# Performance work log

Hardware: AMD Instinct MI355X
Metric: run time of the kernel (lower is better)

Reference implementation:

```python
import jax, jax.numpy as jnp
import numpy as np

B, T, DC, DM, R = 64, 1000, 512, 80, 1
DP = 128          # prenet output dim
DH = 128          # prenet hidden dim
DA = 128          # attention hidden dim
DR = (1024, 1024) # decoder LSTM hidden dims
PZ = 0.1          # zoneout prob (eval-mode mixing)
PD = 0.5          # prenet dropout prob (always on)


def setup_inputs() -> dict:
    key = jax.random.key(0)
    ks = jax.random.split(key, 24)
    s = 0.02  # weight scale to keep activations in a sane range
    inp = {}
    inp['x'] = jax.random.normal(ks[0], (B, R, DM), jnp.float32)
    w = jax.random.uniform(ks[1], (B, T), jnp.float32)
    inp['w'] = w / jnp.sum(w, axis=1, keepdims=True)  # valid attention weights
    inp['h0'] = jax.random.normal(ks[2], (B, DR[0]), jnp.float32) * 0.1
    inp['c0'] = jax.random.normal(ks[3], (B, DR[0]), jnp.float32) * 0.1
    inp['h1'] = jax.random.normal(ks[4], (B, DR[1]), jnp.float32) * 0.1
    inp['c1'] = jax.random.normal(ks[5], (B, DR[1]), jnp.float32) * 0.1
    inp['memory'] = jax.random.normal(ks[6], (B, T, DC), jnp.float32)
    inp['mmask'] = jnp.ones((B, T), dtype=bool)
    inp['pre_w1'] = jax.random.normal(ks[7], (DM * R, DH), jnp.float32) * s
    inp['pre_b1'] = jnp.zeros((DH,), jnp.float32)
    inp['pre_w2'] = jax.random.normal(ks[8], (DH, DP), jnp.float32) * s
    inp['pre_b2'] = jnp.zeros((DP,), jnp.float32)
    inp['wih0'] = jax.random.normal(ks[9], (DP + DC, 4 * DR[0]), jnp.float32) * s
    inp['whh0'] = jax.random.normal(ks[10], (DR[0], 4 * DR[0]), jnp.float32) * s
    inp['b0'] = jnp.zeros((4 * DR[0],), jnp.float32)
    inp['wih1'] = jax.random.normal(ks[11], (DR[0] + DC, 4 * DR[1]), jnp.float32) * s
    inp['whh1'] = jax.random.normal(ks[12], (DR[1], 4 * DR[1]), jnp.float32) * s
    inp['b1'] = jnp.zeros((4 * DR[1],), jnp.float32)
    inp['att_wq'] = jax.random.normal(ks[13], (DR[0] + DR[1] + DC, DA), jnp.float32) * s
    inp['att_wm'] = jax.random.normal(ks[14], (DC, DA), jnp.float32) * s
    inp['att_b'] = jnp.zeros((DA,), jnp.float32)
    inp['att_v'] = jax.random.normal(ks[15], (DA,), jnp.float32) * s
    return inp


def _dropout(v, k, p):
    keep = jax.random.bernoulli(k, 1.0 - p, v.shape)
    return jnp.where(keep, v / (1.0 - p), 0.0)


def _lstm_zoneout(xi, h, c, wih, whh, b):
    # torch LSTMCell gate order: i, f, g, o
    g = xi @ wih + h @ whh + b
    i, f, gg, o = jnp.split(g, 4, axis=1)
    c_new = jax.nn.sigmoid(f) * c + jax.nn.sigmoid(i) * jnp.tanh(gg)
    h_new = jax.nn.sigmoid(o) * jnp.tanh(c_new)
    # eval-mode zoneout: expected-value mixing with previous state
    return (1.0 - PZ) * h_new + PZ * h, (1.0 - PZ) * c_new + PZ * c


def reference(x, w, h0, c0, h1, c1, memory, pre_w1, pre_b1, pre_w2, pre_b2,
              wih0, whh0, b0, wih1, whh1, b1, att_wq, att_wm, att_b, att_v, mmask):
    dk = jax.random.split(jax.random.key(42), 2)
    # PreNet (dropout always on, fixed keys for determinism)
    xf = x.reshape(x.shape[0], -1)                       # [B, r*dim_mel]
    h = _dropout(jax.nn.relu(xf @ pre_w1 + pre_b1), dk[0], PD)
    x_pre = _dropout(jax.nn.relu(h @ pre_w2 + pre_b2), dk[1], PD)  # [B, DP]
    # context = bmm(w, memory)
    ctx = jnp.einsum('bt,btc->bc', w, memory)            # [B, DC]
    # stacked zoneout LSTM cells with interleaved context concat
    h0n, c0n = _lstm_zoneout(jnp.concatenate([x_pre, ctx], axis=1), h0, c0, wih0, whh0, b0)
    h1n, c1n = _lstm_zoneout(jnp.concatenate([h0n, ctx], axis=1), h1, c1, wih1, whh1, b1)
    x_att = jnp.concatenate([h0n, h1n, jnp.zeros_like(ctx)], axis=1)  # [B, 2560]
    # stepwise monotonic attention: e = v.tanh(Wq q + Wm m + b); p = sigmoid(e)
    q = x_att @ att_wq                                   # [B, DA]
    proc = jnp.tanh(q[:, None, :] + jnp.einsum('btc,ca->bta', memory, att_wm) + att_b)
    e = jnp.einsum('bta,a->bt', proc, att_v)             # [B, T]
    e = jnp.where(mmask, e, -1e9)
    p = jax.nn.sigmoid(e)
    # alpha_j = alpha_j * p_j + alpha_{j-1} * (1 - p_{j-1})
    w_new = w * p + jnp.pad((w * (1.0 - p))[:, :-1], ((0, 0), (1, 0)))
    x_dec = jnp.concatenate([h0n, h1n, jnp.zeros_like(ctx)], axis=1)
    return x_dec, ctx, w_new, h0n, c0n, h1n, c1n
```

## Files before the change

kernel.cpp:

```cpp
#include <hip/hip_runtime.h>
#include <hip/hip_bf16.h>
#include <stdint.h>

#define B_  64
#define T_  1000
#define DC_ 512
#define DM_ 80
#define DP_ 128
#define DH_ 128
#define DA_ 128
#define DRN 1024
#define G4  4096

typedef __hip_bfloat16 bf16;
typedef unsigned short u16;
typedef unsigned int   u32;

typedef short bf8_t __attribute__((ext_vector_type(8)));
typedef float f4_t  __attribute__((ext_vector_type(4)));

#define O_XDEC 0
#define O_CTX  163840
#define O_WN   196608
#define O_H0   260608
#define O_C0   326144
#define O_H1   391680
#define O_C1   457216

__device__ __forceinline__ float b2f(bf16 v) { return __bfloat162float(v); }
__device__ __forceinline__ bf16  f2b(float v) { return __float2bfloat16(v); }
__device__ __forceinline__ u16   f2bu(float v) { return __builtin_bit_cast(u16, __float2bfloat16(v)); }

__device__ __forceinline__ float ldv(const float* p, size_t i) { return p[i]; }
__device__ __forceinline__ float ldv(const bf16*  p, size_t i) { return b2f(p[i]); }
__device__ __forceinline__ void  stv(float* p, size_t i, float v) { p[i] = v; }
__device__ __forceinline__ void  stv(bf16*  p, size_t i, float v) { p[i] = f2b(v); }

template<typename T>
__device__ __forceinline__ void ld8f(const T* p, size_t i, float* o) {
    if constexpr (sizeof(T) == 2) {
        uint4 u = *(const uint4*)((const u16*)p + i);
        o[0] = __uint_as_float(u.x << 16); o[1] = __uint_as_float(u.x & 0xffff0000u);
        o[2] = __uint_as_float(u.y << 16); o[3] = __uint_as_float(u.y & 0xffff0000u);
        o[4] = __uint_as_float(u.z << 16); o[5] = __uint_as_float(u.z & 0xffff0000u);
        o[6] = __uint_as_float(u.w << 16); o[7] = __uint_as_float(u.w & 0xffff0000u);
    } else {
        float4 a = *(const float4*)(p + i);
        float4 b = *(const float4*)(p + i + 4);
        o[0]=a.x; o[1]=a.y; o[2]=a.z; o[3]=a.w; o[4]=b.x; o[5]=b.y; o[6]=b.z; o[7]=b.w;
    }
}
__device__ __forceinline__ void ld8f_bits(const u16* p, size_t i, float* o) {
    uint4 u = *(const uint4*)(p + i);
    o[0] = __uint_as_float(u.x << 16); o[1] = __uint_as_float(u.x & 0xffff0000u);
    o[2] = __uint_as_float(u.y << 16); o[3] = __uint_as_float(u.y & 0xffff0000u);
    o[4] = __uint_as_float(u.z << 16); o[5] = __uint_as_float(u.z & 0xffff0000u);
    o[6] = __uint_as_float(u.w << 16); o[7] = __uint_as_float(u.w & 0xffff0000u);
}

__device__ __forceinline__ bool sniff_is_f32(const u32* h0raw) {
    int lane = threadIdx.x & 63;
    int c = 0;
    #pragma unroll
    for (int i = 0; i < 4; ++i) {
        u32 e = (h0raw[lane * 4 + i] >> 7) & 0xFF;
        c += (e >= 100 && e <= 126) ? 1 : 0;
    }
    #pragma unroll
    for (int s = 1; s < 64; s <<= 1) c += __shfl_xor(c, s);
    return c < 128;
}

__device__ __forceinline__ u32 rotl32(u32 v, int r) { return (v << r) | (v >> (32 - r)); }
__device__ __forceinline__ void threefry2x32(u32 k0, u32 k1, u32 x0, u32 x1, u32& y0, u32& y1) {
    u32 ks2 = k0 ^ k1 ^ 0x1BD11BDAu;
    x0 += k0; x1 += k1;
#define TF_R(r) { x0 += x1; x1 = rotl32(x1, r); x1 ^= x0; }
    TF_R(13) TF_R(15) TF_R(26) TF_R(6)
    x0 += k1; x1 += ks2 + 1u;
    TF_R(17) TF_R(29) TF_R(16) TF_R(24)
    x0 += ks2; x1 += k0 + 2u;
    TF_R(13) TF_R(15) TF_R(26) TF_R(6)
    x0 += k0; x1 += k1 + 3u;
    TF_R(17) TF_R(29) TF_R(16) TF_R(24)
    x0 += k1; x1 += ks2 + 4u;
    TF_R(13) TF_R(15) TF_R(26) TF_R(6)
    x0 += ks2; x1 += k0 + 5u;
#undef TF_R
    y0 = x0; y1 = x1;
}
__device__ __forceinline__ float dropout_mask(int which, int j) {
    u32 dk0, dk1, b1, b2;
    threefry2x32(0u, 42u, 0u, (u32)which, dk0, dk1);
    threefry2x32(dk0, dk1, 0u, (u32)j, b1, b2);
    u32 bits = b1 ^ b2;
    float u = __uint_as_float((bits >> 9) | 0x3f800000u) - 1.0f;
    return (u < 0.5f) ? 2.0f : 0.0f;
}

template<typename T>
__device__ void prep_impl(const T* wm, u16* BTwm,
                          const T* x, const T* w1, const T* pb1, const T* w2, const T* pb2,
                          u16* Ab0, float* shbuf) {
    int bid = blockIdx.x, tid = threadIdx.x;
    if (bid < 32) {
        int gid = bid * 256 + tid;
        int L = gid & 63, kc = (gid >> 6) & 15, at = gid >> 10;
        u16* dst = BTwm + (size_t)gid * 8;
        int col = at * 16 + (L & 15);
        int krow = kc * 32 + (L >> 4) * 8;
        u16 v[8];
        #pragma unroll
        for (int j = 0; j < 8; ++j) v[j] = f2bu(ldv(wm, (size_t)(krow + j) * DA_ + col));
        uint4 pk;
        pk.x = v[0] | ((u32)v[1] << 16); pk.y = v[2] | ((u32)v[3] << 16);
        pk.z = v[4] | ((u32)v[5] << 16); pk.w = v[6] | ((u32)v[7] << 16);
        *(uint4*)dst = pk;
    } else {
        int b = bid - 32;
        float* xs = shbuf;
        float* hs = shbuf + DM_;
        if (tid < DM_) xs[tid] = ldv(x, (size_t)b * DM_ + tid);
        __syncthreads();
        if (tid < DH_) {
            float acc = ldv(pb1, tid);
            #pragma unroll 8
            for (int k = 0; k < DM_; ++k) acc = fmaf(xs[k], ldv(w1, (size_t)k * DH_ + tid), acc);
            acc = fmaxf(acc, 0.f) * dropout_mask(0, b * DH_ + tid);
            hs[tid] = acc;
        }
        __syncthreads();
        if (tid < DP_) {
            float acc2 = ldv(pb2, tid);
            #pragma unroll 8
            for (int k = 0; k < DH_; ++k) acc2 = fmaf(hs[k], ldv(w2, (size_t)k * DP_ + tid), acc2);
            acc2 = fmaxf(acc2, 0.f) * dropout_mask(1, b * DP_ + tid);
            Ab0[(size_t)b * 1664 + tid] = f2bu(acc2);
        }
    }
}
__global__ __launch_bounds__(256) void prep_kernel(const u32* h0r,
        const void* wm, u16* BTwm,
        const void* x, const void* w1, const void* pb1, const void* w2, const void* pb2,
        u16* Ab0) {
    __shared__ float shbuf[DM_ + DH_];
    if (sniff_is_f32(h0r))
        prep_impl<float>((const float*)wm, BTwm, (const float*)x,
                         (const float*)w1, (const float*)pb1, (const float*)w2, (const float*)pb2, Ab0, shbuf);
    else
        prep_impl<bf16>((const bf16*)wm, BTwm, (const bf16*)x,
                        (const bf16*)w1, (const bf16*)pb1, (const bf16*)w2, (const bf16*)pb2, Ab0, shbuf);
}

template<typename T>
__device__ void ctxproj_impl(const T* mem, const T* w, const u16* BTwm,
                             float* CTXP, u16* Mproj, u16* Alds, float* shw) {
    int tid = threadIdx.x;
    int t0 = blockIdx.x * 128, b = blockIdx.y;
    if (tid < 128) shw[tid] = (t0 + tid < T_) ? ldv(w, (size_t)b * T_ + t0 + tid) : 0.f;
    int L = tid & 63;
    int m = L & 15, q16 = L >> 4;
    int wat = tid >> 6;
    int rg = tid >> 5, cg = tid & 31;

    bf8_t bw[16];
    #pragma unroll
    for (int kc = 0; kc < 16; ++kc)
        bw[kc] = *(const bf8_t*)(BTwm + ((size_t)(wat * 16 + kc) * 64 + L) * 8);

    f4_t acc[4];
    #pragma unroll
    for (int mt = 0; mt < 4; ++mt) acc[mt] = (f4_t){0.f, 0.f, 0.f, 0.f};
    float cacc[16] = {};
    uint4  stb[4];
    float4 stf[8];

#define LOADSTEP(S) do {                                                         \
        const int tt_ = (S) >> 1, ph_ = (S) & 1;                                 \
        _Pragma("unroll")                                                        \
        for (int rr = 0; rr < 4; ++rr) {                                         \
            int i = rr * 512 + tid;                                              \
            int row = i >> 5, c16 = i & 31;                                      \
            int t = t0 + tt_ * 64 + row;                                         \
            size_t base = (size_t)(b * T_ + ((t < T_) ? t : 0)) * DC_ + ph_ * 256 + c16 * 8; \
            if constexpr (sizeof(T) == 2) {                                      \
                stb[rr] = (t < T_) ? *(const uint4*)((const u16*)mem + base)     \
                                   : make_uint4(0u, 0u, 0u, 0u);                 \
            } else {                                                             \
                if (t < T_) { stf[2*rr]   = *(const float4*)(mem + base);        \
                              stf[2*rr+1] = *(const float4*)(mem + base + 4); }  \
                else { stf[2*rr] = make_float4(0.f,0.f,0.f,0.f);                 \
                       stf[2*rr+1] = make_float4(0.f,0.f,0.f,0.f); }             \
            }                                                                    \
        }                                                                        \
    } while (0)

    LOADSTEP(0);
    #pragma unroll
    for (int step = 0; step < 4; ++step) {
        const int tt = step >> 1, ph = step & 1;
        __syncthreads();
        #pragma unroll
        for (int rr = 0; rr < 4; ++rr) {
            int i = rr * 512 + tid;
            int row = i >> 5, c16 = i & 31;
            float wvv = shw[tt * 64 + row];
            uint4 v;
            if constexpr (sizeof(T) == 2) {
                v = stb[rr];
                float f0 = __uint_as_float(v.x << 16), f1 = __uint_as_float(v.x & 0xffff0000u);
                float f2 = __uint_as_float(v.y << 16), f3 = __uint_as_float(v.y & 0xffff0000u);
                float f4 = __uint_as_float(v.z << 16), f5 = __uint_as_float(v.z & 0xffff0000u);
                float f6 = __uint_as_float(v.w << 16), f7 = __uint_as_float(v.w & 0xffff0000u);
                cacc[ph*8+0] = fmaf(wvv, f0, cacc[ph*8+0]); cacc[ph*8+1] = fmaf(wvv, f1, cacc[ph*8+1]);
                cacc[ph*8+2] = fmaf(wvv, f2, cacc[ph*8+2]); cacc[ph*8+3] = fmaf(wvv, f3, cacc[ph*8+3]);
                cacc[ph*8+4] = fmaf(wvv, f4, cacc[ph*8+4]); cacc[ph*8+5] = fmaf(wvv, f5, cacc[ph*8+5]);
                cacc[ph*8+6] = fmaf(wvv, f6, cacc[ph*8+6]); cacc[ph*8+7] = fmaf(wvv, f7, cacc[ph*8+7]);
            } else {
                float4 a = stf[2*rr], bb = stf[2*rr+1];
                cacc[ph*8+0] = fmaf(wvv, a.x,  cacc[ph*8+0]); cacc[ph*8+1] = fmaf(wvv, a.y,  cacc[ph*8+1]);
                cacc[ph*8+2] = fmaf(wvv, a.z,  cacc[ph*8+2]); cacc[ph*8+3] = fmaf(wvv, a.w,  cacc[ph*8+3]);
                cacc[ph*8+4] = fmaf(wvv, bb.x, cacc[ph*8+4]); cacc[ph*8+5] = fmaf(wvv, bb.y, cacc[ph*8+5]);
                cacc[ph*8+6] = fmaf(wvv, bb.z, cacc[ph*8+6]); cacc[ph*8+7] = fmaf(wvv, bb.w, cacc[ph*8+7]);
                v.x = (u32)f2bu(a.x)  | ((u32)f2bu(a.y)  << 16);
                v.y = (u32)f2bu(a.z)  | ((u32)f2bu(a.w)  << 16);
                v.z = (u32)f2bu(bb.x) | ((u32)f2bu(bb.y) << 16);
                v.w = (u32)f2bu(bb.z) | ((u32)f2bu(bb.w) << 16);
            }
            *(uint4*)(Alds + row * 264 + c16 * 8) = v;
        }
        __syncthreads();
        if (step == 0) LOADSTEP(1);
        else if (step == 1) LOADSTEP(2);
        else if (step == 2) LOADSTEP(3);
        #pragma unroll
        for (int kcl = 0; kcl < 8; ++kcl) {
            const int kc = ph * 8 + kcl;
            #pragma unroll
            for (int mt = 0; mt < 4; ++mt) {
                bf8_t af = *(const bf8_t*)(Alds + (mt * 16 + m) * 264 + kcl * 32 + q16 * 8);
                acc[mt] = __builtin_amdgcn_mfma_f32_16x16x32_bf16(af, bw[kc], acc[mt], 0, 0, 0);
            }
        }
        if (ph == 1) {
            #pragma unroll
            for (int mt = 0; mt < 4; ++mt) {
                #pragma unroll
                for (int r = 0; r < 4; ++r) {
                    int trow = t0 + tt * 64 + mt * 16 + q16 * 4 + r;
                    if (trow < T_)
                        Mproj[(size_t)(b * T_ + trow) * DA_ + wat * 16 + m] = f2bu(acc[mt][r]);
                }
                acc[mt] = (f4_t){0.f, 0.f, 0.f, 0.f};
            }
        }
    }
#undef LOADSTEP
    __syncthreads();
    float* part = (float*)Alds;
    #pragma unroll
    for (int ph = 0; ph < 2; ++ph)
        #pragma unroll
        for (int j = 0; j < 8; ++j)
            part[rg * 512 + ph * 256 + cg * 8 + j] = cacc[ph * 8 + j];
    __syncthreads();
    int c = tid;
    float s = 0.f;
    #pragma unroll
    for (int gg = 0; gg < 16; ++gg) s += part[gg * 512 + c];
    CTXP[((size_t)blockIdx.x * 64 + b) * DC_ + c] = s;
}
__global__ __launch_bounds__(512, 1) void ctxproj_bf16_kernel(const u32* h0r,
        const void* mem, const void* w, const u16* BTwm, float* CTXP, u16* Mproj) {
    __shared__ __align__(16) u16 Alds[64 * 264];
    __shared__ float shw[128];
    if (sniff_is_f32(h0r)) return;
    ctxproj_impl<bf16>((const bf16*)mem, (const bf16*)w, BTwm, CTXP, Mproj, Alds, shw);
}
__global__ __launch_bounds__(512, 1) void ctxproj_f32_kernel(const u32* h0r,
        const void* mem, const void* w, const u16* BTwm, float* CTXP, u16* Mproj) {
    __shared__ __align__(16) u16 Alds[64 * 264];
    __shared__ float shw[128];
    if (!sniff_is_f32(h0r)) return;
    ctxproj_impl<float>((const float*)mem, (const float*)w, BTwm, CTXP, Mproj, Alds, shw);
}

template<typename T>
__device__ void pack0_impl(const float* CTXP, const T* h0p, const T* h1p,
                           u16* Ab0, u16* Ab1, float* QPf, T* out) {
    int b = blockIdx.x, tid = threadIdx.x;
    T* ctxout = out + O_CTX;
    T* xdec = out + O_XDEC;
    if (tid < 128) QPf[(size_t)b * DA_ + tid] = 0.f;
    for (int c = tid; c < DC_; c += 256) {
        float s = 0.f;
        #pragma unroll
        for (int t = 0; t < 8; ++t) s += CTXP[((size_t)t * 64 + b) * DC_ + c];
        u16 bv = f2bu(s);
        Ab0[(size_t)b * 1664 + 128 + c] = bv;
        Ab1[(size_t)b * 2560 + 1024 + c] = bv;
        stv(ctxout, (size_t)b * DC_ + c, s);
        stv(xdec, (size_t)b * 2560 + 2048 + c, 0.f);
    }
    for (int u = tid; u < DRN; u += 256) {
        Ab0[(size_t)b * 1664 + 640 + u]  = f2bu(ldv(h0p, (size_t)b * DRN + u));
        Ab1[(size_t)b * 2560 + 1536 + u] = f2bu(ldv(h1p, (size_t)b * DRN + u));
    }
}
__global__ __launch_bounds__(256) void pack0_kernel(const u32* h0r, const float* CTXP,
        const void* h0p, const void* h1p, u16* Ab0, u16* Ab1, float* QPf, void* out) {
    if (sniff_is_f32(h0r))
        pack0_impl<float>(CTXP, (const float*)h0p, (const float*)h1p, Ab0, Ab1, QPf, (float*)out);
    else
        pack0_impl<bf16>(CTXP, (const bf16*)h0p, (const bf16*)h1p, Ab0, Ab1, QPf, (bf16*)out);
}

template<typename T>
__device__ void gemm_impl(const u16* Abuf, int K, int L12, const T* Wih, const T* Whh,
                          float* Gs, int nchunks, float (*As)[66], float (*Ws)[64]) {
    int tid = threadIdx.x;
    int n0b = blockIdx.x * 64;
    int kbase = blockIdx.y * (nchunks * 64);
    int cx = tid & 15, ry = tid >> 4;
    int b0 = ry * 4, n0 = cx * 4;
    int a_bb = tid >> 2, a_k16 = (tid & 3) * 16;
    int w_k  = tid >> 2, w_n16 = (tid & 3) * 16;
    float acc[4][4] = {};
    float va[16], vw[16];
#define GLOAD(CH) do {                                                          \
        int k0 = kbase + (CH) * 64;                                             \
        ld8f_bits(Abuf, (size_t)a_bb * K + k0 + a_k16, va);                     \
        ld8f_bits(Abuf, (size_t)a_bb * K + k0 + a_k16 + 8, va + 8);             \
        int kg = k0 + w_k;                                                      \
        const T* wr = (kg < L12) ? (Wih + (size_t)kg * G4) : (Whh + (size_t)(kg - L12) * G4); \
        ld8f(wr, n0b + w_n16, vw);                                              \
        ld8f(wr, n0b + w_n16 + 8, vw + 8);                                      \
    } while (0)
    GLOAD(0);
    for (int ch = 0; ch < nchunks; ++ch) {
        __syncthreads();
        #pragma unroll
        for (int j = 0; j < 16; ++j) As[a_bb][a_k16 + j] = va[j];
        #pragma unroll
        for (int j = 0; j < 16; ++j) Ws[w_k][w_n16 + j] = vw[j];
        __syncthreads();
        if (ch + 1 < nchunks) GLOAD(ch + 1);
        #pragma unroll
        for (int kk = 0; kk < 64; kk += 2) {
            float2 av[4];
            #pragma unroll
            for (int r = 0; r < 4; ++r) av[r] = *(const float2*)&As[b0 + r][kk];
            float4 w0 = *(const float4*)&Ws[kk][n0];
            float4 w1 = *(const float4*)&Ws[kk + 1][n0];
            #pragma unroll
            for (int r = 0; r < 4; ++r) {
                acc[r][0] = fmaf(av[r].x, w0.x, acc[r][0]); acc[r][0] = fmaf(av[r].y, w1.x, acc[r][0]);
                acc[r][1] = fmaf(av[r].x, w0.y, acc[r][1]); acc[r][1] = fmaf(av[r].y, w1.y, acc[r][1]);
                acc[r][2] = fmaf(av[r].x, w0.z, acc[r][2]); acc[r][2] = fmaf(av[r].y, w1.z, acc[r][2]);
                acc[r][3] = fmaf(av[r].x, w0.w, acc[r][3]); acc[r][3] = fmaf(av[r].y, w1.w, acc[r][3]);
            }
        }
    }
#undef GLOAD
    float* outp = Gs + (size_t)blockIdx.y * (64 * G4);
    #pragma unroll
    for (int r = 0; r < 4; ++r)
        *(float4*)&outp[(size_t)(b0 + r) * G4 + n0b + n0] =
            make_float4(acc[r][0], acc[r][1], acc[r][2], acc[r][3]);
}
__global__ __launch_bounds__(256) void gemm_kernel(const u32* h0r, const u16* Abuf,
        int K, int L12, const void* Wih, const void* Whh, float* Gs, int nchunks) {
    __shared__ float As[64][66];
    __shared__ float Ws[64][64];
    if (sniff_is_f32(h0r))
        gemm_impl<float>(Abuf, K, L12, (const float*)Wih, (const float*)Whh, Gs, nchunks, As, Ws);
    else
        gemm_impl<bf16>(Abuf, K, L12, (const bf16*)Wih, (const bf16*)Whh, Gs, nchunks, As, Ws);
}

template<typename T>
__device__ void gate_impl(const float* Gs, int nsplit, const T* bias, const T* hprev,
                          const T* cprev, const T* wq, int qrow0, float* QPf,
                          T* out, int ho_off, int co_off, int xoff, u16* Ab1,
                          float* hos, float* sarr) {
    int tid = threadIdx.x;
    int idx = blockIdx.x * 256 + tid;
    int b = idx >> 10, u = idx & 1023;
    int u0 = (blockIdx.x & 3) * 256;
    float gi = ldv(bias, u);
    float gf = ldv(bias, 1024 + u);
    float gg = ldv(bias, 2048 + u);
    float go = ldv(bias, 3072 + u);
    for (int s = 0; s < nsplit; ++s) {
        const float* g = Gs + (size_t)s * (64 * G4) + (size_t)b * G4;
        gi += g[u]; gf += g[1024 + u]; gg += g[2048 + u]; go += g[3072 + u];
    }
    float c = ldv(cprev, idx), h = ldv(hprev, idx);
    float si = 1.f / (1.f + expf(-gi));
    float sf = 1.f / (1.f + expf(-gf));
    float so = 1.f / (1.f + expf(-go));
    float cn = sf * c + si * tanhf(gg);
    float hn = so * tanhf(cn);
    float ho = 0.9f * hn + 0.1f * h;
    float co = 0.9f * cn + 0.1f * c;
    stv(out + ho_off, idx, ho);
    stv(out + co_off, idx, co);
    stv(out + O_XDEC, (size_t)b * 2560 + xoff + u, ho);
    if (Ab1 != nullptr) Ab1[(size_t)b * 2560 + u] = f2bu(ho);
    hos[tid] = ho;
    __syncthreads();
    int a = tid & 127, half = tid >> 7;
    float s = 0.f;
    #pragma unroll 8
    for (int j = 0; j < 128; ++j)
        s = fmaf(hos[half * 128 + j], ldv(wq, (size_t)(qrow0 + u0 + half * 128 + j) * DA_ + a), s);
    sarr[tid] = s;
    __syncthreads();
    if (tid < 128) atomicAdd(&QPf[(size_t)b * DA_ + tid], sarr[tid] + sarr[128 + tid]);
}
__global__ __launch_bounds__(256) void gate_kernel(const u32* h0r, const float* Gs, int nsplit,
        const void* bias, const void* hprev, const void* cprev, const void* wq, int qrow0,
        float* QPf, void* out, int ho_off, int co_off, int xoff, u16* Ab1) {
    __shared__ float hos[256];
    __shared__ float sarr[256];
    if (sniff_is_f32(h0r))
        gate_impl<float>(Gs, nsplit, (const float*)bias, (const float*)hprev, (const float*)cprev,
                         (const float*)wq, qrow0, QPf, (float*)out, ho_off, co_off, xoff, Ab1, hos, sarr);
    else
        gate_impl<bf16>(Gs, nsplit, (const bf16*)bias, (const bf16*)hprev, (const bf16*)cprev,
                        (const bf16*)wq, qrow0, QPf, (bf16*)out, ho_off, co_off, xoff, Ab1, hos, sarr);
}

template<typename T>
__device__ void attn_impl(const u16* Mproj, const float* QPf, const T* ab, const T* av,
                          const T* w, T* out, float* qa, float* avl, float* psh) {
    int tid = threadIdx.x;
    int t0 = blockIdx.x * 64, b = blockIdx.y;
    T* wout = out + O_WN;
    if (tid < DA_) {
        qa[tid]  = ldv(ab, tid) + QPf[(size_t)b * DA_ + tid];
        avl[tid] = ldv(av, tid);
    }
    __syncthreads();
    int quad = tid & 3, r = tid >> 2;
    #pragma unroll
    for (int rbase = 0; rbase < 2; ++rbase) {
        int rrow = (rbase == 0) ? r : 64;
        bool act = (rbase == 0) || (r == 0);
        int t = t0 - 1 + rrow;
        float e = 0.f;
        if (act && t >= 0 && t < T_) {
            #pragma unroll
            for (int a8 = 0; a8 < 4; ++a8) {
                float v[8];
                ld8f_bits(Mproj, (size_t)(b * T_ + t) * DA_ + quad * 32 + a8 * 8, v);
                #pragma unroll
                for (int j = 0; j < 8; ++j) {
                    int a = quad * 32 + a8 * 8 + j;
                    e = fmaf(avl[a], tanhf(qa[a] + v[j]), e);
                }
            }
        }
        e += __shfl_xor(e, 1);
        e += __shfl_xor(e, 2);
        if (act && quad == 0 && t >= 0 && t < T_) psh[rrow] = 1.f / (1.f + expf(-e));
    }
    __syncthreads();
    if (tid < 64) {
        int t = t0 + tid;
        if (t < T_) {
            float val = ldv(w, (size_t)b * T_ + t) * psh[tid + 1];
            if (t > 0) val = fmaf(ldv(w, (size_t)b * T_ + t - 1), 1.f - psh[tid], val);
            stv(wout, (size_t)b * T_ + t, val);
        }
    }
}
__global__ __launch_bounds__(256) void attn_kernel(const u32* h0r, const u16* Mproj,
        const float* QPf, const void* ab, const void* av, const void* w, void* out) {
    __shared__ float qa[DA_];
    __shared__ float avl[DA_];
    __shared__ float psh[66];
    if (sniff_is_f32(h0r))
        attn_impl<float>(Mproj, QPf, (const float*)ab, (const float*)av, (const float*)w,
                         (float*)out, qa, avl, psh);
    else
        attn_impl<bf16>(Mproj, QPf, (const bf16*)ab, (const bf16*)av, (const bf16*)w,
                        (bf16*)out, qa, avl, psh);
}

extern "C" void kernel_launch(void* const* d_in, const int* in_sizes, int n_in,
                              void* d_out, int out_size, void* d_ws, size_t ws_size,
                              hipStream_t stream) {
    (void)in_sizes; (void)n_in; (void)out_size; (void)ws_size;

    float* wsf   = (float*)d_ws;
    float* GS    = wsf;
    float* CTXP  = wsf + 4194304;
    float* QPf   = wsf + 4718592;
    u16*   MPROJ = (u16*)(wsf + 4784128);
    u16*   AB0   = (u16*)(wsf + 8880128);
    u16*   AB1   = (u16*)(wsf + 8933376);
    u16*   BTWM  = (u16*)(wsf + 9080832);

    const u32* H0R = (const u32*)d_in[2];

    prep_kernel<<<96, 256, 0, stream>>>(H0R, d_in[19], BTWM,
                                        d_in[0], d_in[8], d_in[9], d_in[10], d_in[11], AB0);
    ctxproj_bf16_kernel<<<dim3(8, 64), 512, 0, stream>>>(H0R, d_in[6], d_in[1], BTWM, CTXP, MPROJ);
    ctxproj_f32_kernel <<<dim3(8, 64), 512, 0, stream>>>(H0R, d_in[6], d_in[1], BTWM, CTXP, MPROJ);
    pack0_kernel<<<64, 256, 0, stream>>>(H0R, CTXP, d_in[2], d_in[4], AB0, AB1, QPf, d_out);
    gemm_kernel<<<dim3(64, 13), 256, 0, stream>>>(H0R, AB0, 1664, 640, d_in[12], d_in[13], GS, 2);
    gate_kernel<<<256, 256, 0, stream>>>(H0R, GS, 13, d_in[14], d_in[2], d_in[3],
                                         d_in[18], 0, QPf, d_out, O_H0, O_C0, 0, AB1);
    gemm_kernel<<<dim3(64, 10), 256, 0, stream>>>(H0R, AB1, 2560, 1536, d_in[15], d_in[16], GS, 4);
    gate_kernel<<<256, 256, 0, stream>>>(H0R, GS, 10, d_in[17], d_in[4], d_in[5],
                                         d_in[18], 1024, QPf, d_out, O_H1, O_C1, 1024, (u16*)nullptr);
    attn_kernel<<<dim3(16, 64), 256, 0, stream>>>(H0R, MPROJ, QPf, d_in[20], d_in[21], d_in[1], d_out);
}
```

Baseline: 384.5 us.

## Precompute recurrent h@Whh GEMMs in prep kernel and double-buffer ctxproj loads

```diff
diff --git a/kernel.cpp b/kernel.cpp
--- a/kernel.cpp
+++ b/kernel.cpp
@@ -11,6 +11,7 @@
 #define DA_ 128
 #define DRN 1024
 #define G4  4096
+#define SPLIT 262144
 
 typedef __hip_bfloat16 bf16;
 typedef unsigned short u16;
@@ -99,9 +100,64 @@
 }
 
 template<typename T>
+__device__ void hgemm_impl(const T* hprev, const T* Whh, float* GsL, int unit,
+                           float (*As)[66], float (*Ws)[64]) {
+    int tid = threadIdx.x;
+    int n0b = (unit & 63) * 64;
+    int split = unit >> 6;
+    int kbase = split * 256;
+    int cx = tid & 15, ry = tid >> 4;
+    int b0 = ry * 4, n0 = cx * 4;
+    int a_bb = tid >> 2, a_k16 = (tid & 3) * 16;
+    int w_k  = tid >> 2, w_n16 = (tid & 3) * 16;
+    float acc[4][4] = {};
+    float va[16], vw[16];
+#define HGLOAD(CH) do {                                                         \
+        int k0 = kbase + (CH) * 64;                                             \
+        ld8f(hprev, (size_t)a_bb * DRN + k0 + a_k16, va);                       \
+        ld8f(hprev, (size_t)a_bb * DRN + k0 + a_k16 + 8, va + 8);               \
+        const T* wr = Whh + (size_t)(k0 + w_k) * G4;                            \
+        ld8f(wr, n0b + w_n16, vw);                                              \
+        ld8f(wr, n0b + w_n16 + 8, vw + 8);                                      \
+    } while (0)
+    HGLOAD(0);
+    for (int ch = 0; ch < 4; ++ch) {
+        __syncthreads();
+        #pragma unroll
+        for (int j = 0; j < 16; ++j) As[a_bb][a_k16 + j] = va[j];
+        #pragma unroll
+        for (int j = 0; j < 16; ++j) Ws[w_k][w_n16 + j] = vw[j];
+        __syncthreads();
+        if (ch + 1 < 4) HGLOAD(ch + 1);
+        #pragma unroll
+        for (int kk = 0; kk < 64; kk += 2) {
+            float2 av[4];
+            #pragma unroll
+            for (int r = 0; r < 4; ++r) av[r] = *(const float2*)&As[b0 + r][kk];
+            float4 w0 = *(const float4*)&Ws[kk][n0];
+            float4 w1 = *(const float4*)&Ws[kk + 1][n0];
+            #pragma unroll
+            for (int r = 0; r < 4; ++r) {
+                acc[r][0] = fmaf(av[r].x, w0.x, acc[r][0]); acc[r][0] = fmaf(av[r].y, w1.x, acc[r][0]);
+                acc[r][1] = fmaf(av[r].x, w0.y, acc[r][1]); acc[r][1] = fmaf(av[r].y, w1.y, acc[r][1]);
+                acc[r][2] = fmaf(av[r].x, w0.z, acc[r][2]); acc[r][2] = fmaf(av[r].y, w1.z, acc[r][2]);
+                acc[r][3] = fmaf(av[r].x, w0.w, acc[r][3]); acc[r][3] = fmaf(av[r].y, w1.w, acc[r][3]);
+            }
+        }
+    }
+#undef HGLOAD
+    float* outp = GsL + (size_t)split * (64 * G4);
+    #pragma unroll
+    for (int r = 0; r < 4; ++r)
+        *(float4*)&outp[(size_t)(b0 + r) * G4 + n0b + n0] =
+            make_float4(acc[r][0], acc[r][1], acc[r][2], acc[r][3]);
+}
+
+template<typename T>
 __device__ void prep_impl(const T* wm, u16* BTwm,
                           const T* x, const T* w1, const T* pb1, const T* w2, const T* pb2,
-                          u16* Ab0, float* shbuf) {
+                          u16* Ab0, const T* h0p, const T* whh0, const T* h1p, const T* whh1,
+                          float* GS, float (*As)[66], float (*Ws)[64]) {
     int bid = blockIdx.x, tid = threadIdx.x;
     if (bid < 32) {
         int gid = bid * 256 + tid;
@@ -116,10 +172,10 @@
         pk.x = v[0] | ((u32)v[1] << 16); pk.y = v[2] | ((u32)v[3] << 16);
         pk.z = v[4] | ((u32)v[5] << 16); pk.w = v[6] | ((u32)v[7] << 16);
         *(uint4*)dst = pk;
-    } else {
+    } else if (bid < 96) {
         int b = bid - 32;
-        float* xs = shbuf;
-        float* hs = shbuf + DM_;
+        float* xs = &As[0][0];
+        float* hs = xs + DM_;
         if (tid < DM_) xs[tid] = ldv(x, (size_t)b * DM_ + tid);
         __syncthreads();
         if (tid < DH_) {
@@ -137,19 +193,29 @@
             acc2 = fmaxf(acc2, 0.f) * dropout_mask(1, b * DP_ + tid);
             Ab0[(size_t)b * 1664 + tid] = f2bu(acc2);
         }
+    } else if (bid < 352) {
+        hgemm_impl<T>(h0p, whh0, GS, bid - 96, As, Ws);
+    } else {
+        hgemm_impl<T>(h1p, whh1, GS + (size_t)6 * SPLIT, bid - 352, As, Ws);
     }
 }
 __global__ __launch_bounds__(256) void prep_kernel(const u32* h0r,
         const void* wm, u16* BTwm,
         const void* x, const void* w1, const void* pb1, const void* w2, const void* pb2,
-        u16* Ab0) {
-    __shared__ float shbuf[DM_ + DH_];
+        u16* Ab0, const void* h0p, const void* whh0, const void* h1p, const void* whh1,
+        float* GS) {
+    __shared__ float As[64][66];
+    __shared__ float Ws[64][64];
     if (sniff_is_f32(h0r))
         prep_impl<float>((const float*)wm, BTwm, (const float*)x,
-                         (const float*)w1, (const float*)pb1, (const float*)w2, (const float*)pb2, Ab0, shbuf);
+                         (const float*)w1, (const float*)pb1, (const float*)w2, (const float*)pb2,
+                         Ab0, (const float*)h0p, (const float*)whh0, (const float*)h1p,
+                         (const float*)whh1, GS, As, Ws);
     else
         prep_impl<bf16>((const bf16*)wm, BTwm, (const bf16*)x,
-                        (const bf16*)w1, (const bf16*)pb1, (const bf16*)w2, (const bf16*)pb2, Ab0, shbuf);
+                        (const bf16*)w1, (const bf16*)pb1, (const bf16*)w2, (const bf16*)pb2,
+                        Ab0, (const bf16*)h0p, (const bf16*)whh0, (const bf16*)h1p,
+                        (const bf16*)whh1, GS, As, Ws);
 }
 
 template<typename T>
@@ -172,10 +238,10 @@
     #pragma unroll
     for (int mt = 0; mt < 4; ++mt) acc[mt] = (f4_t){0.f, 0.f, 0.f, 0.f};
     float cacc[16] = {};
-    uint4  stb[4];
-    float4 stf[8];
-
-#define LOADSTEP(S) do {                                                         \
+    uint4  stbA[4], stbB[4];
+    float4 stfA[8], stfB[8];
+
+#define LOADSTEP(S, STB, STF) do {                                               \
         const int tt_ = (S) >> 1, ph_ = (S) & 1;                                 \
         _Pragma("unroll")                                                        \
         for (int rr = 0; rr < 4; ++rr) {                                         \
@@ -184,78 +250,100 @@
             int t = t0 + tt_ * 64 + row;                                         \
             size_t base = (size_t)(b * T_ + ((t < T_) ? t : 0)) * DC_ + ph_ * 256 + c16 * 8; \
             if constexpr (sizeof(T) == 2) {                                      \
-                stb[rr] = (t < T_) ? *(const uint4*)((const u16*)mem + base)     \
+                STB[rr] = (t < T_) ? *(const uint4*)((const u16*)mem + base)     \
                                    : make_uint4(0u, 0u, 0u, 0u);                 \
             } else {                                                             \
-                if (t < T_) { stf[2*rr]   = *(const float4*)(mem + base);        \
-                              stf[2*rr+1] = *(const float4*)(mem + base + 4); }  \
-                else { stf[2*rr] = make_float4(0.f,0.f,0.f,0.f);                 \
-                       stf[2*rr+1] = make_float4(0.f,0.f,0.f,0.f); }             \
+                if (t < T_) { STF[2*rr]   = *(const float4*)(mem + base);        \
+                              STF[2*rr+1] = *(const float4*)(mem + base + 4); }  \
+                else { STF[2*rr] = make_float4(0.f,0.f,0.f,0.f);                 \
+                       STF[2*rr+1] = make_float4(0.f,0.f,0.f,0.f); }             \
             }                                                                    \
         }                                                                        \
     } while (0)
 
-    LOADSTEP(0);
-    #pragma unroll
-    for (int step = 0; step < 4; ++step) {
-        const int tt = step >> 1, ph = step & 1;
-        __syncthreads();
-        #pragma unroll
-        for (int rr = 0; rr < 4; ++rr) {
-            int i = rr * 512 + tid;
-            int row = i >> 5, c16 = i & 31;
-            float wvv = shw[tt * 64 + row];
-            uint4 v;
-            if constexpr (sizeof(T) == 2) {
-                v = stb[rr];
-                float f0 = __uint_as_float(v.x << 16), f1 = __uint_as_float(v.x & 0xffff0000u);
-                float f2 = __uint_as_float(v.y << 16), f3 = __uint_as_float(v.y & 0xffff0000u);
-                float f4 = __uint_as_float(v.z << 16), f5 = __uint_as_float(v.z & 0xffff0000u);
-                float f6 = __uint_as_float(v.w << 16), f7 = __uint_as_float(v.w & 0xffff0000u);
-                cacc[ph*8+0] = fmaf(wvv, f0, cacc[ph*8+0]); cacc[ph*8+1] = fmaf(wvv, f1, cacc[ph*8+1]);
-                cacc[ph*8+2] = fmaf(wvv, f2, cacc[ph*8+2]); cacc[ph*8+3] = fmaf(wvv, f3, cacc[ph*8+3]);
-                cacc[ph*8+4] = fmaf(wvv, f4, cacc[ph*8+4]); cacc[ph*8+5] = fmaf(wvv, f5, cacc[ph*8+5]);
-                cacc[ph*8+6] = fmaf(wvv, f6, cacc[ph*8+6]); cacc[ph*8+7] = fmaf(wvv, f7, cacc[ph*8+7]);
-            } else {
-                float4 a = stf[2*rr], bb = stf[2*rr+1];
-                cacc[ph*8+0] = fmaf(wvv, a.x,  cacc[ph*8+0]); cacc[ph*8+1] = fmaf(wvv, a.y,  cacc[ph*8+1]);
-                cacc[ph*8+2] = fmaf(wvv, a.z,  cacc[ph*8+2]); cacc[ph*8+3] = fmaf(wvv, a.w,  cacc[ph*8+3]);
-                cacc[ph*8+4] = fmaf(wvv, bb.x, cacc[ph*8+4]); cacc[ph*8+5] = fmaf(wvv, bb.y, cacc[ph*8+5]);
-                cacc[ph*8+6] = fmaf(wvv, bb.z, cacc[ph*8+6]); cacc[ph*8+7] = fmaf(wvv, bb.w, cacc[ph*8+7]);
-                v.x = (u32)f2bu(a.x)  | ((u32)f2bu(a.y)  << 16);
-                v.y = (u32)f2bu(a.z)  | ((u32)f2bu(a.w)  << 16);
-                v.z = (u32)f2bu(bb.x) | ((u32)f2bu(bb.y) << 16);
-                v.w = (u32)f2bu(bb.z) | ((u32)f2bu(bb.w) << 16);
-            }
-            *(uint4*)(Alds + row * 264 + c16 * 8) = v;
-        }
-        __syncthreads();
-        if (step == 0) LOADSTEP(1);
-        else if (step == 1) LOADSTEP(2);
-        else if (step == 2) LOADSTEP(3);
-        #pragma unroll
-        for (int kcl = 0; kcl < 8; ++kcl) {
-            const int kc = ph * 8 + kcl;
-            #pragma unroll
-            for (int mt = 0; mt < 4; ++mt) {
-                bf8_t af = *(const bf8_t*)(Alds + (mt * 16 + m) * 264 + kcl * 32 + q16 * 8);
-                acc[mt] = __builtin_amdgcn_mfma_f32_16x16x32_bf16(af, bw[kc], acc[mt], 0, 0, 0);
-            }
-        }
-        if (ph == 1) {
-            #pragma unroll
-            for (int mt = 0; mt < 4; ++mt) {
-                #pragma unroll
-                for (int r = 0; r < 4; ++r) {
-                    int trow = t0 + tt * 64 + mt * 16 + q16 * 4 + r;
-                    if (trow < T_)
-                        Mproj[(size_t)(b * T_ + trow) * DA_ + wat * 16 + m] = f2bu(acc[mt][r]);
-                }
-                acc[mt] = (f4_t){0.f, 0.f, 0.f, 0.f};
-            }
-        }
-    }
+#define WRITESTEP(TT, PH, STB, STF) do {                                         \
+        _Pragma("unroll")                                                        \
+        for (int rr = 0; rr < 4; ++rr) {                                         \
+            int i = rr * 512 + tid;                                              \
+            int row = i >> 5, c16 = i & 31;                                      \
+            float wvv = shw[(TT) * 64 + row];                                    \
+            uint4 v;                                                             \
+            if constexpr (sizeof(T) == 2) {                                      \
+                v = STB[rr];                                                     \
+                float f0 = __uint_as_float(v.x << 16), f1 = __uint_as_float(v.x & 0xffff0000u); \
+                float f2 = __uint_as_float(v.y << 16), f3 = __uint_as_float(v.y & 0xffff0000u); \
+                float f4 = __uint_as_float(v.z << 16), f5 = __uint_as_float(v.z & 0xffff0000u); \
+                float f6 = __uint_as_float(v.w << 16), f7 = __uint_as_float(v.w & 0xffff0000u); \
+                cacc[(PH)*8+0] = fmaf(wvv, f0, cacc[(PH)*8+0]); cacc[(PH)*8+1] = fmaf(wvv, f1, cacc[(PH)*8+1]); \
+                cacc[(PH)*8+2] = fmaf(wvv, f2, cacc[(PH)*8+2]); cacc[(PH)*8+3] = fmaf(wvv, f3, cacc[(PH)*8+3]); \
+                cacc[(PH)*8+4] = fmaf(wvv, f4, cacc[(PH)*8+4]); cacc[(PH)*8+5] = fmaf(wvv, f5, cacc[(PH)*8+5]); \
+                cacc[(PH)*8+6] = fmaf(wvv, f6, cacc[(PH)*8+6]); cacc[(PH)*8+7] = fmaf(wvv, f7, cacc[(PH)*8+7]); \
+            } else {                                                             \
+                float4 a = STF[2*rr], bb = STF[2*rr+1];                          \
+                cacc[(PH)*8+0] = fmaf(wvv, a.x,  cacc[(PH)*8+0]); cacc[(PH)*8+1] = fmaf(wvv, a.y,  cacc[(PH)*8+1]); \
+                cacc[(PH)*8+2] = fmaf(wvv, a.z,  cacc[(PH)*8+2]); cacc[(PH)*8+3] = fmaf(wvv, a.w,  cacc[(PH)*8+3]); \
+                cacc[(PH)*8+4] = fmaf(wvv, bb.x, cacc[(PH)*8+4]); cacc[(PH)*8+5] = fmaf(wvv, bb.y, cacc[(PH)*8+5]); \
+                cacc[(PH)*8+6] = fmaf(wvv, bb.z, cacc[(PH)*8+6]); cacc[(PH)*8+7] = fmaf(wvv, bb.w, cacc[(PH)*8+7]); \
+                v.x = (u32)f2bu(a.x)  | ((u32)f2bu(a.y)  << 16);                 \
+                v.y = (u32)f2bu(a.z)  | ((u32)f2bu(a.w)  << 16);                 \
+                v.z = (u32)f2bu(bb.x) | ((u32)f2bu(bb.y) << 16);                 \
+                v.w = (u32)f2bu(bb.z) | ((u32)f2bu(bb.w) << 16);                 \
+            }                                                                    \
+            *(uint4*)(Alds + row * 264 + c16 * 8) = v;                           \
+        }                                                                        \
+    } while (0)
+
+#define COMPUTESTEP(PH) do {                                                     \
+        _Pragma("unroll")                                                        \
+        for (int kcl = 0; kcl < 8; ++kcl) {                                      \
+            const int kc = (PH) * 8 + kcl;                                       \
+            _Pragma("unroll")                                                    \
+            for (int mt = 0; mt < 4; ++mt) {                                     \
+                bf8_t af = *(const bf8_t*)(Alds + (mt * 16 + m) * 264 + kcl * 32 + q16 * 8); \
+                acc[mt] = __builtin_amdgcn_mfma_f32_16x16x32_bf16(af, bw[kc], acc[mt], 0, 0, 0); \
+            }                                                                    \
+        }                                                                        \
+    } while (0)
+
+#define MPROJSTORE(TT) do {                                                      \
+        _Pragma("unroll")                                                        \
+        for (int mt = 0; mt < 4; ++mt) {                                         \
+            _Pragma("unroll")                                                    \
+            for (int r = 0; r < 4; ++r) {                                        \
+                int trow = t0 + (TT) * 64 + mt * 16 + q16 * 4 + r;               \
+                if (trow < T_)                                                   \
+                    Mproj[(size_t)(b * T_ + trow) * DA_ + wat * 16 + m] = f2bu(acc[mt][r]); \
+            }                                                                    \
+            acc[mt] = (f4_t){0.f, 0.f, 0.f, 0.f};                                \
+        }                                                                        \
+    } while (0)
+
+    LOADSTEP(0, stbA, stfA);
+    LOADSTEP(1, stbB, stfB);
+    __syncthreads();
+    WRITESTEP(0, 0, stbA, stfA);
+    __syncthreads();
+    LOADSTEP(2, stbA, stfA);
+    COMPUTESTEP(0);
+    __syncthreads();
+    WRITESTEP(0, 1, stbB, stfB);
+    __syncthreads();
+    LOADSTEP(3, stbB, stfB);
+    COMPUTESTEP(1);
+    MPROJSTORE(0);
+    __syncthreads();
+    WRITESTEP(1, 0, stbA, stfA);
+    __syncthreads();
+    COMPUTESTEP(0);
+    __syncthreads();
+    WRITESTEP(1, 1, stbB, stfB);
+    __syncthreads();
+    COMPUTESTEP(1);
+    MPROJSTORE(1);
 #undef LOADSTEP
+#undef WRITESTEP
+#undef COMPUTESTEP
+#undef MPROJSTORE
     __syncthreads();
     float* part = (float*)Alds;
     #pragma unroll
@@ -286,8 +374,7 @@
 }
 
 template<typename T>
-__device__ void pack0_impl(const float* CTXP, const T* h0p, const T* h1p,
-                           u16* Ab0, u16* Ab1, float* QPf, T* out) {
+__device__ void pack0_impl(const float* CTXP, u16* Ab0, u16* Ab1, float* QPf, T* out) {
     int b = blockIdx.x, tid = threadIdx.x;
     T* ctxout = out + O_CTX;
     T* xdec = out + O_XDEC;
@@ -302,17 +389,13 @@
         stv(ctxout, (size_t)b * DC_ + c, s);
         stv(xdec, (size_t)b * 2560 + 2048 + c, 0.f);
     }
-    for (int u = tid; u < DRN; u += 256) {
-        Ab0[(size_t)b * 1664 + 640 + u]  = f2bu(ldv(h0p, (size_t)b * DRN + u));
-        Ab1[(size_t)b * 2560 + 1536 + u] = f2bu(ldv(h1p, (size_t)b * DRN + u));
-    }
 }
 __global__ __launch_bounds__(256) void pack0_kernel(const u32* h0r, const float* CTXP,
-        const void* h0p, const void* h1p, u16* Ab0, u16* Ab1, float* QPf, void* out) {
+        u16* Ab0, u16* Ab1, float* QPf, void* out) {
     if (sniff_is_f32(h0r))
-        pack0_impl<float>(CTXP, (const float*)h0p, (const float*)h1p, Ab0, Ab1, QPf, (float*)out);
+        pack0_impl<float>(CTXP, Ab0, Ab1, QPf, (float*)out);
     else
-        pack0_impl<bf16>(CTXP, (const bf16*)h0p, (const bf16*)h1p, Ab0, Ab1, QPf, (bf16*)out);
+        pack0_impl<bf16>(CTXP, Ab0, Ab1, QPf, (bf16*)out);
 }
 
 template<typename T>
@@ -504,16 +587,19 @@
 
     const u32* H0R = (const u32*)d_in[2];
 
-    prep_kernel<<<96, 256, 0, stream>>>(H0R, d_in[19], BTWM,
-                                        d_in[0], d_in[8], d_in[9], d_in[10], d_in[11], AB0);
+    prep_kernel<<<608, 256, 0, stream>>>(H0R, d_in[19], BTWM,
+                                         d_in[0], d_in[8], d_in[9], d_in[10], d_in[11], AB0,
+                                         d_in[2], d_in[13], d_in[4], d_in[16], GS);
     ctxproj_bf16_kernel<<<dim3(8, 64), 512, 0, stream>>>(H0R, d_in[6], d_in[1], BTWM, CTXP, MPROJ);
     ctxproj_f32_kernel <<<dim3(8, 64), 512, 0, stream>>>(H0R, d_in[6], d_in[1], BTWM, CTXP, MPROJ);
-    pack0_kernel<<<64, 256, 0, stream>>>(H0R, CTXP, d_in[2], d_in[4], AB0, AB1, QPf, d_out);
-    gemm_kernel<<<dim3(64, 13), 256, 0, stream>>>(H0R, AB0, 1664, 640, d_in[12], d_in[13], GS, 2);
-    gate_kernel<<<256, 256, 0, stream>>>(H0R, GS, 13, d_in[14], d_in[2], d_in[3],
+    pack0_kernel<<<64, 256, 0, stream>>>(H0R, CTXP, AB0, AB1, QPf, d_out);
+    gemm_kernel<<<dim3(64, 2), 256, 0, stream>>>(H0R, AB0, 1664, 640, d_in[12], d_in[12],
+                                                 GS + (size_t)4 * SPLIT, 5);
+    gate_kernel<<<256, 256, 0, stream>>>(H0R, GS, 6, d_in[14], d_in[2], d_in[3],
                                          d_in[18], 0, QPf, d_out, O_H0, O_C0, 0, AB1);
-    gemm_kernel<<<dim3(64, 10), 256, 0, stream>>>(H0R, AB1, 2560, 1536, d_in[15], d_in[16], GS, 4);
-    gate_kernel<<<256, 256, 0, stream>>>(H0R, GS, 10, d_in[17], d_in[4], d_in[5],
+    gemm_kernel<<<dim3(64, 3), 256, 0, stream>>>(H0R, AB1, 2560, 1536, d_in[15], d_in[15],
+                                                 GS + (size_t)10 * SPLIT, 8);
+    gate_kernel<<<256, 256, 0, stream>>>(H0R, GS + (size_t)6 * SPLIT, 7, d_in[17], d_in[4], d_in[5],
                                          d_in[18], 1024, QPf, d_out, O_H1, O_C1, 1024, (u16*)nullptr);
     attn_kernel<<<dim3(16, 64), 256, 0, stream>>>(H0R, MPROJ, QPf, d_in[20], d_in[21], d_in[1], d_out);
 }
```

After: 388.8 us. About the same (+1.1%).
